# Optimization experiments

Measured on AMD Instinct MI355X. Metric: run time of the kernel, lower is better.

Reference implementation:

```python
import jax, jax.numpy as jnp
import numpy as np

N_NODES = 50000
N_EDGES = 800000
HIDDEN = 128
BN_EPS = 1e-5


def setup_inputs() -> dict:
    key = jax.random.key(0)
    k_h, k_e, k_wl, k_wr = jax.random.split(key, 4)
    h = jax.random.normal(k_h, (N_NODES, HIDDEN), dtype=jnp.float32)
    edge_index = jax.random.randint(k_e, (2, N_EDGES), 0, N_NODES, dtype=jnp.int32)
    W_l = jax.random.normal(k_wl, (HIDDEN, HIDDEN), dtype=jnp.float32) / np.sqrt(HIDDEN)
    b_l = jnp.zeros((HIDDEN,), dtype=jnp.float32)
    W_r = jax.random.normal(k_wr, (HIDDEN, HIDDEN), dtype=jnp.float32) / np.sqrt(HIDDEN)
    gamma = jnp.ones((HIDDEN,), dtype=jnp.float32)
    beta = jnp.zeros((HIDDEN,), dtype=jnp.float32)
    return {"h": h, "edge_index": edge_index, "W_l": W_l, "b_l": b_l,
            "W_r": W_r, "gamma": gamma, "beta": beta}


def reference(h, edge_index, W_l, b_l, W_r, gamma, beta):
    # SAGEConv(aggr='mean'): out_i = W_l @ mean_{j->i} h_j + b_l + W_r @ h_i
    src = edge_index[0]  # message sources
    dst = edge_index[1]  # message targets
    n = h.shape[0]
    msg_sum = jax.ops.segment_sum(h[src], dst, num_segments=n)          # [N, D]
    deg = jax.ops.segment_sum(jnp.ones_like(dst, dtype=h.dtype), dst, num_segments=n)
    agg = msg_sum / jnp.maximum(deg, 1.0)[:, None]                      # mean aggregation
    out = agg @ W_l.T + b_l + h @ W_r.T                                 # [N, D]
    # BatchNorm1d (training mode: batch statistics, biased variance)
    mean = jnp.mean(out, axis=0)
    var = jnp.var(out, axis=0)
    out = gamma * (out - mean) * jax.lax.rsqrt(var + BN_EPS) + beta
    out = jax.nn.relu(out)
    # dropout p=0.0 -> identity; residual add
    return out + h
```

## Files before the change

kernel.cpp:

```cpp
#include <hip/hip_runtime.h>

#define N_NODES 50000
#define N_EDGES 800000
#define HIDDEN  128
#define BN_EPS  1e-5f

typedef __attribute__((ext_vector_type(8))) short short8;
typedef __attribute__((ext_vector_type(8))) unsigned short ushort8;
typedef __attribute__((ext_vector_type(4))) float f32x4;

#define NBS 196

__device__ inline unsigned short f2bf(float x) {
    unsigned u = __float_as_uint(x);
    return (unsigned short)((u + 0x7FFFu + ((u >> 16) & 1u)) >> 16);
}
__device__ inline float bf2f(unsigned short u) {
    return __uint_as_float(((unsigned)u) << 16);
}
__device__ inline void cvt8(const float* x, short8& hi, short8& lo) {
#pragma unroll
    for (int i = 0; i < 8; i++) {
        unsigned u = __float_as_uint(x[i]);
        unsigned r = (u + 0x7FFFu + ((u >> 16) & 1u)) & 0xFFFF0000u;
        hi[i] = (short)(r >> 16);
        lo[i] = (short)f2bf(x[i] - __uint_as_float(r));
    }
}

#define NB_EDGE 3125
#define NB_HB   3125
#define NB_W    128

__global__ __launch_bounds__(256) void prep_kernel(
    const int* __restrict__ edge_index,
    const float* __restrict__ h,
    const float* __restrict__ W_l,
    const float* __restrict__ W_r,
    int* __restrict__ cnt,
    unsigned short* __restrict__ hb,
    unsigned short* __restrict__ WhiG,
    unsigned short* __restrict__ WloG,
    float* __restrict__ bn_acc)
{
    const int b = blockIdx.x;
    const int tid = threadIdx.x;
    if (b < NB_EDGE) {
        const int e = b * 256 + tid;
        atomicAdd(&cnt[edge_index[N_EDGES + e]], 1);
    } else if (b < NB_EDGE + NB_HB) {
        if (b == NB_EDGE) bn_acc[tid] = 0.0f;
        const size_t i8 = ((size_t)(b - NB_EDGE) * 256 + tid) * 8;
        const float4 p0 = *reinterpret_cast<const float4*>(h + i8);
        const float4 p1 = *reinterpret_cast<const float4*>(h + i8 + 4);
        ushort8 v;
        v[0] = f2bf(p0.x); v[1] = f2bf(p0.y); v[2] = f2bf(p0.z); v[3] = f2bf(p0.w);
        v[4] = f2bf(p1.x); v[5] = f2bf(p1.y); v[6] = f2bf(p1.z); v[7] = f2bf(p1.w);
        *reinterpret_cast<ushort8*>(hb + i8) = v;
    } else {
        const int gid = (b - NB_EDGE - NB_HB) * 256 + tid;
        const int n = gid >> 8;
        const int k = gid & 255;
        const float w = (k < 128) ? W_l[n * 128 + k] : W_r[n * 128 + (k - 128)];
        unsigned u = __float_as_uint(w);
        unsigned r = (u + 0x7FFFu + ((u >> 16) & 1u)) & 0xFFFF0000u;
        WhiG[gid] = (unsigned short)(r >> 16);
        WloG[gid] = f2bf(w - __uint_as_float(r));
    }
}

__global__ __launch_bounds__(256) void scan1_kernel(
    const int* __restrict__ cnt,
    int* __restrict__ bsum)
{
    const int t = threadIdx.x;
    const int idx = blockIdx.x * 256 + t;
    int v = (idx < N_NODES) ? cnt[idx] : 0;
    __shared__ int ps[256];
    ps[t] = v;
    __syncthreads();
    for (int off = 128; off > 0; off >>= 1) {
        if (t < off) ps[t] += ps[t + off];
        __syncthreads();
    }
    if (t == 0) bsum[blockIdx.x] = ps[0];
}

__global__ __launch_bounds__(256) void scan2_kernel(
    const int* __restrict__ bsum,
    int* __restrict__ boff,
    int* __restrict__ rp)
{
    const int t = threadIdx.x;
    int v = (t < NBS) ? bsum[t] : 0;
    __shared__ int ps[256];
    ps[t] = v;
    __syncthreads();
    for (int off = 1; off < 256; off <<= 1) {
        const int u = (t >= off) ? ps[t - off] : 0;
        __syncthreads();
        ps[t] += u;
        __syncthreads();
    }
    if (t < NBS) boff[t] = ps[t] - v;
    if (t == 255) rp[N_NODES] = ps[255];
}

__global__ __launch_bounds__(256) void scan3_kernel(
    const int* __restrict__ cnt,
    const int* __restrict__ boff,
    int* __restrict__ rp)
{
    const int t = threadIdx.x;
    const int idx = blockIdx.x * 256 + t;
    const int v = (idx < N_NODES) ? cnt[idx] : 0;
    __shared__ int ps[256];
    ps[t] = v;
    __syncthreads();
    for (int off = 1; off < 256; off <<= 1) {
        const int u = (t >= off) ? ps[t - off] : 0;
        __syncthreads();
        ps[t] += u;
        __syncthreads();
    }
    if (idx < N_NODES) rp[idx] = boff[blockIdx.x] + ps[t] - v;
}

__global__ __launch_bounds__(256) void place_kernel(
    const int* __restrict__ edge_index,
    const int* __restrict__ rp,
    int* __restrict__ cnt,
    unsigned short* __restrict__ csr)
{
    const int e = blockIdx.x * 256 + threadIdx.x;
    const int d = edge_index[N_EDGES + e];
    const int s = edge_index[e];
    const int pos = atomicSub(&cnt[d], 1) - 1;
    csr[rp[d] + pos] = (unsigned short)s;
}

__global__ __launch_bounds__(256) void gather_kernel(
    const unsigned short* __restrict__ hb,
    const int* __restrict__ rp,
    const unsigned short* __restrict__ csr,
    unsigned short* __restrict__ aggb)
{
    const int group = (threadIdx.x >> 4) & 3;
    const int sub   = threadIdx.x & 15;
    const int wave  = (blockIdx.x * 256 + threadIdx.x) >> 6;
    const int n = wave * 4 + group;
    if (n >= N_NODES) return;

    const int base = rp[n];
    const int c = rp[n + 1] - base;
    const int fo = sub * 8;

    float acc[8];
#pragma unroll
    for (int i = 0; i < 8; i++) acc[i] = 0.0f;

    int j = 0;
    for (; j + 4 <= c; j += 4) {
        const int s0 = csr[base + j],     s1 = csr[base + j + 1];
        const int s2 = csr[base + j + 2], s3 = csr[base + j + 3];
        const ushort8 v0 = *reinterpret_cast<const ushort8*>(hb + (size_t)s0 * HIDDEN + fo);
        const ushort8 v1 = *reinterpret_cast<const ushort8*>(hb + (size_t)s1 * HIDDEN + fo);
        const ushort8 v2 = *reinterpret_cast<const ushort8*>(hb + (size_t)s2 * HIDDEN + fo);
        const ushort8 v3 = *reinterpret_cast<const ushort8*>(hb + (size_t)s3 * HIDDEN + fo);
#pragma unroll
        for (int i = 0; i < 8; i++)
            acc[i] += (bf2f(v0[i]) + bf2f(v1[i])) + (bf2f(v2[i]) + bf2f(v3[i]));
    }
    for (; j < c; j++) {
        const ushort8 v0 = *reinterpret_cast<const ushort8*>(hb + (size_t)csr[base + j] * HIDDEN + fo);
#pragma unroll
        for (int i = 0; i < 8; i++) acc[i] += bf2f(v0[i]);
    }
    const float inv = 1.0f / (float)((c > 0) ? c : 1);
    ushort8 o;
#pragma unroll
    for (int i = 0; i < 8; i++) o[i] = f2bf(acc[i] * inv);
    *reinterpret_cast<ushort8*>(aggb + (size_t)n * HIDDEN + fo) = o;
}

__global__ __launch_bounds__(256) void gemm_kernel(
    const unsigned short* __restrict__ aggb,
    const float* __restrict__ h,
    const unsigned short* __restrict__ WhiG,
    const unsigned short* __restrict__ WloG,
    const float* __restrict__ b_l,
    float* __restrict__ out,
    float* __restrict__ bn_acc)
{
    __shared__ short WsH[128][64];
    __shared__ short WsL[128][64];
    __shared__ float bnS[128];
    __shared__ float bnS2[128];

    const int tid  = threadIdx.x;
    const int lane = tid & 63;
    const int wv   = tid >> 6;
    const int row0 = blockIdx.x * 128;
    const int colb = lane & 15;
    const int quad = lane >> 4;

    if (tid < 128) { bnS[tid] = 0.0f; bnS2[tid] = 0.0f; }

    f32x4 acc[2][8];
#pragma unroll
    for (int s = 0; s < 2; s++)
#pragma unroll
        for (int c = 0; c < 8; c++) acc[s][c] = (f32x4)(0.0f);

    const int wcol  = tid >> 1;
    const int sbase = (tid & 1) * 4;

    for (int kc = 0; kc < 4; kc++) {
        const int kb = (kc & 1) * 64;
        const int kw = kc * 64;

        __syncthreads();
#pragma unroll
        for (int j = 0; j < 4; j++) {
            const int slot = sbase + j;
            short8 vh = *reinterpret_cast<const short8*>(WhiG + (size_t)wcol * 256 + kw + slot * 8);
            short8 vl = *reinterpret_cast<const short8*>(WloG + (size_t)wcol * 256 + kw + slot * 8);
            const int sp = slot ^ (wcol & 7);
            *reinterpret_cast<short8*>(&WsH[wcol][sp * 8]) = vh;
            *reinterpret_cast<short8*>(&WsL[wcol][sp * 8]) = vl;
        }
        __syncthreads();

#pragma unroll
        for (int ks = 0; ks < 2; ks++) {
            short8 ahi[2], alo[2];
#pragma unroll
            for (int sub = 0; sub < 2; sub++) {
                int row = row0 + wv * 32 + sub * 16 + colb;
                row = (row < N_NODES) ? row : (N_NODES - 1);
                if (kc < 2) {
                    ahi[sub] = *reinterpret_cast<const short8*>(
                        aggb + (size_t)row * HIDDEN + kb + ks * 32 + quad * 8);
                } else {
                    const float* xp = h + (size_t)row * HIDDEN + kb + ks * 32 + quad * 8;
                    float xr[8];
                    const float4 p0 = *reinterpret_cast<const float4*>(xp);
                    const float4 p1 = *reinterpret_cast<const float4*>(xp + 4);
                    xr[0] = p0.x; xr[1] = p0.y; xr[2] = p0.z; xr[3] = p0.w;
                    xr[4] = p1.x; xr[5] = p1.y; xr[6] = p1.z; xr[7] = p1.w;
                    cvt8(xr, ahi[sub], alo[sub]);
                }
            }
#pragma unroll
            for (int c = 0; c < 8; c++) {
                const int bc = c * 16 + colb;
                const int sp = (ks * 4 + quad) ^ (bc & 7);
                short8 bhi = *reinterpret_cast<const short8*>(&WsH[bc][sp * 8]);
                short8 blo = *reinterpret_cast<const short8*>(&WsL[bc][sp * 8]);
#pragma unroll
                for (int sub = 0; sub < 2; sub++) {
                    acc[sub][c] = __builtin_amdgcn_mfma_f32_16x16x32_bf16(ahi[sub], bhi, acc[sub][c], 0, 0, 0);
                    acc[sub][c] = __builtin_amdgcn_mfma_f32_16x16x32_bf16(ahi[sub], blo, acc[sub][c], 0, 0, 0);
                    if (kc >= 2)
                        acc[sub][c] = __builtin_amdgcn_mfma_f32_16x16x32_bf16(alo[sub], bhi, acc[sub][c], 0, 0, 0);
                }
            }
        }
    }

#pragma unroll
    for (int c = 0; c < 8; c++) {
        const int col = c * 16 + colb;
        const float bias = b_l[col];
        float s = 0.0f, s2 = 0.0f;
#pragma unroll
        for (int sub = 0; sub < 2; sub++) {
            const int rbase = row0 + wv * 32 + sub * 16 + quad * 4;
#pragma unroll
            for (int reg = 0; reg < 4; reg++) {
                const int r = rbase + reg;
                if (r < N_NODES) {
                    const float o = acc[sub][c][reg] + bias;
                    out[(size_t)r * HIDDEN + col] = o;
                    s += o; s2 += o * o;
                }
            }
        }
        atomicAdd(&bnS[col], s);
        atomicAdd(&bnS2[col], s2);
    }
    __syncthreads();
    if (tid < 128) {
        atomicAdd(&bn_acc[tid], bnS[tid]);
        atomicAdd(&bn_acc[128 + tid], bnS2[tid]);
    }
}

__global__ __launch_bounds__(256) void bn_apply_kernel(
    const float* __restrict__ h,
    const float* __restrict__ gamma,
    const float* __restrict__ beta,
    const float* __restrict__ bn_acc,
    float* __restrict__ out)
{
    const float inv_n = 1.0f / (float)N_NODES;
    const size_t total = (size_t)N_NODES * HIDDEN;
    size_t idx = ((size_t)blockIdx.x * blockDim.x + threadIdx.x) * 4;
    const size_t stride = (size_t)gridDim.x * blockDim.x * 4;

    for (; idx < total; idx += stride) {
        const int col = (int)(idx & (HIDDEN - 1));
        float4 x  = *reinterpret_cast<float4*>(out + idx);
        float4 sm = *reinterpret_cast<const float4*>(bn_acc + col);
        float4 sq = *reinterpret_cast<const float4*>(bn_acc + HIDDEN + col);
        float4 g  = *reinterpret_cast<const float4*>(gamma + col);
        float4 bt = *reinterpret_cast<const float4*>(beta + col);
        float4 hr = *reinterpret_cast<const float4*>(h + idx);

        float4 res;
        {
            float m = sm.x * inv_n; float var = sq.x * inv_n - m * m;
            float v = g.x * (x.x - m) * rsqrtf(var + BN_EPS) + bt.x;
            res.x = fmaxf(v, 0.0f) + hr.x;
        }
        {
            float m = sm.y * inv_n; float var = sq.y * inv_n - m * m;
            float v = g.y * (x.y - m) * rsqrtf(var + BN_EPS) + bt.y;
            res.y = fmaxf(v, 0.0f) + hr.y;
        }
        {
            float m = sm.z * inv_n; float var = sq.z * inv_n - m * m;
            float v = g.z * (x.z - m) * rsqrtf(var + BN_EPS) + bt.z;
            res.z = fmaxf(v, 0.0f) + hr.z;
        }
        {
            float m = sm.w * inv_n; float var = sq.w * inv_n - m * m;
            float v = g.w * (x.w - m) * rsqrtf(var + BN_EPS) + bt.w;
            res.w = fmaxf(v, 0.0f) + hr.w;
        }
        *reinterpret_cast<float4*>(out + idx) = res;
    }
}

extern "C" void kernel_launch(void* const* d_in, const int* in_sizes, int n_in,
                              void* d_out, int out_size, void* d_ws, size_t ws_size,
                              hipStream_t stream)
{
    const float* h          = (const float*)d_in[0];
    const int*   edge_index = (const int*)d_in[1];
    const float* W_l        = (const float*)d_in[2];
    const float* b_l        = (const float*)d_in[3];
    const float* W_r        = (const float*)d_in[4];
    const float* gamma      = (const float*)d_in[5];
    const float* beta       = (const float*)d_in[6];
    float* out = (float*)d_out;

    char* ws = (char*)d_ws;
    int* cnt  = (int*)ws;
    int* rp   = cnt + 50000;
    int* bsum = rp + 50004;
    int* boff = bsum + 256;
    unsigned short* csr  = (unsigned short*)(boff + 256);
    unsigned short* hb   = csr + 800000;
    unsigned short* aggb = hb + 6400000;
    unsigned short* WhiG = aggb + 6400000;
    unsigned short* WloG = WhiG + 32768;
    float* bn_acc = (float*)(WloG + 32768);

    hipMemsetAsync(cnt, 0, 50000 * sizeof(int), stream);

    prep_kernel<<<NB_EDGE + NB_HB + NB_W, 256, 0, stream>>>(
        edge_index, h, W_l, W_r, cnt, hb, WhiG, WloG, bn_acc);

    scan1_kernel<<<NBS, 256, 0, stream>>>(cnt, bsum);
    scan2_kernel<<<1, 256, 0, stream>>>(bsum, boff, rp);
    scan3_kernel<<<NBS, 256, 0, stream>>>(cnt, boff, rp);

    place_kernel<<<NB_EDGE, 256, 0, stream>>>(edge_index, rp, cnt, csr);

    gather_kernel<<<(N_NODES / 4 + 3) / 4, 256, 0, stream>>>(hb, rp, csr, aggb);

    gemm_kernel<<<(N_NODES + 127) / 128, 256, 0, stream>>>(
        aggb, h, WhiG, WloG, b_l, out, bn_acc);

    bn_apply_kernel<<<2048, 256, 0, stream>>>(h, gamma, beta, bn_acc, out);
}
```

Measured before the change: 250.4 us.

## Fuse scan stages into one kernel and halve GEMM row tile per block

Merges the single-block block-offset scan and the per-block prefix scan into one kernel. Each block redundantly scans the 196 block sums, which removes one launch and the boff round trip through global memory. Also shrinks the GEMM tile from 128 to 64 rows per block, so each wave handles one 16-row subtile and the grid doubles to about 782 blocks. This improves occupancy and load balance on the many CUs, but doubles how often the weight tiles are staged into shared memory and the number of BN atomics.

```diff
diff --git a/kernel.cpp b/kernel.cpp
--- a/kernel.cpp
+++ b/kernel.cpp
@@ -86,32 +86,26 @@
     if (t == 0) bsum[blockIdx.x] = ps[0];
 }
 
-__global__ __launch_bounds__(256) void scan2_kernel(
+__global__ __launch_bounds__(256) void scan23_kernel(
+    const int* __restrict__ cnt,
     const int* __restrict__ bsum,
-    int* __restrict__ boff,
     int* __restrict__ rp)
 {
     const int t = threadIdx.x;
-    int v = (t < NBS) ? bsum[t] : 0;
-    __shared__ int ps[256];
-    ps[t] = v;
+    __shared__ int bs[256];
+    const int bv = (t < NBS) ? bsum[t] : 0;
+    bs[t] = bv;
     __syncthreads();
     for (int off = 1; off < 256; off <<= 1) {
-        const int u = (t >= off) ? ps[t - off] : 0;
-        __syncthreads();
-        ps[t] += u;
-        __syncthreads();
-    }
-    if (t < NBS) boff[t] = ps[t] - v;
-    if (t == 255) rp[N_NODES] = ps[255];
-}
-
-__global__ __launch_bounds__(256) void scan3_kernel(
-    const int* __restrict__ cnt,
-    const int* __restrict__ boff,
-    int* __restrict__ rp)
-{
-    const int t = threadIdx.x;
+        const int u = (t >= off) ? bs[t - off] : 0;
+        __syncthreads();
+        bs[t] += u;
+        __syncthreads();
+    }
+    if (blockIdx.x == 0 && t == 255) rp[N_NODES] = bs[255];
+    const int boff = bs[blockIdx.x] - bsum[blockIdx.x];
+    __syncthreads();
+
     const int idx = blockIdx.x * 256 + t;
     const int v = (idx < N_NODES) ? cnt[idx] : 0;
     __shared__ int ps[256];
@@ -123,7 +117,7 @@
         ps[t] += u;
         __syncthreads();
     }
-    if (idx < N_NODES) rp[idx] = boff[blockIdx.x] + ps[t] - v;
+    if (idx < N_NODES) rp[idx] = boff + ps[t] - v;
 }
 
 __global__ __launch_bounds__(256) void place_kernel(
@@ -200,17 +194,15 @@
     const int tid  = threadIdx.x;
     const int lane = tid & 63;
     const int wv   = tid >> 6;
-    const int row0 = blockIdx.x * 128;
+    const int row0 = blockIdx.x * 64;
     const int colb = lane & 15;
     const int quad = lane >> 4;
 
     if (tid < 128) { bnS[tid] = 0.0f; bnS2[tid] = 0.0f; }
 
-    f32x4 acc[2][8];
-#pragma unroll
-    for (int s = 0; s < 2; s++)
-#pragma unroll
-        for (int c = 0; c < 8; c++) acc[s][c] = (f32x4)(0.0f);
+    f32x4 acc[8];
+#pragma unroll
+    for (int c = 0; c < 8; c++) acc[c] = (f32x4)(0.0f);
 
     const int wcol  = tid >> 1;
     const int sbase = (tid & 1) * 4;
@@ -233,13 +225,12 @@
 
 #pragma unroll
         for (int ks = 0; ks < 2; ks++) {
-            short8 ahi[2], alo[2];
-#pragma unroll
-            for (int sub = 0; sub < 2; sub++) {
-                int row = row0 + wv * 32 + sub * 16 + colb;
+            short8 ahi, alo;
+            {
+                int row = row0 + wv * 16 + colb;
                 row = (row < N_NODES) ? row : (N_NODES - 1);
                 if (kc < 2) {
-                    ahi[sub] = *reinterpret_cast<const short8*>(
+                    ahi = *reinterpret_cast<const short8*>(
                         aggb + (size_t)row * HIDDEN + kb + ks * 32 + quad * 8);
                 } else {
                     const float* xp = h + (size_t)row * HIDDEN + kb + ks * 32 + quad * 8;
@@ -248,7 +239,7 @@
                     const float4 p1 = *reinterpret_cast<const float4*>(xp + 4);
                     xr[0] = p0.x; xr[1] = p0.y; xr[2] = p0.z; xr[3] = p0.w;
                     xr[4] = p1.x; xr[5] = p1.y; xr[6] = p1.z; xr[7] = p1.w;
-                    cvt8(xr, ahi[sub], alo[sub]);
+                    cvt8(xr, ahi, alo);
                 }
             }
 #pragma unroll
@@ -257,13 +248,10 @@
                 const int sp = (ks * 4 + quad) ^ (bc & 7);
                 short8 bhi = *reinterpret_cast<const short8*>(&WsH[bc][sp * 8]);
                 short8 blo = *reinterpret_cast<const short8*>(&WsL[bc][sp * 8]);
-#pragma unroll
-                for (int sub = 0; sub < 2; sub++) {
-                    acc[sub][c] = __builtin_amdgcn_mfma_f32_16x16x32_bf16(ahi[sub], bhi, acc[sub][c], 0, 0, 0);
-                    acc[sub][c] = __builtin_amdgcn_mfma_f32_16x16x32_bf16(ahi[sub], blo, acc[sub][c], 0, 0, 0);
-                    if (kc >= 2)
-                        acc[sub][c] = __builtin_amdgcn_mfma_f32_16x16x32_bf16(alo[sub], bhi, acc[sub][c], 0, 0, 0);
-                }
+                acc[c] = __builtin_amdgcn_mfma_f32_16x16x32_bf16(ahi, bhi, acc[c], 0, 0, 0);
+                acc[c] = __builtin_amdgcn_mfma_f32_16x16x32_bf16(ahi, blo, acc[c], 0, 0, 0);
+                if (kc >= 2)
+                    acc[c] = __builtin_amdgcn_mfma_f32_16x16x32_bf16(alo, bhi, acc[c], 0, 0, 0);
             }
         }
     }
@@ -273,17 +261,14 @@
         const int col = c * 16 + colb;
         const float bias = b_l[col];
         float s = 0.0f, s2 = 0.0f;
-#pragma unroll
-        for (int sub = 0; sub < 2; sub++) {
-            const int rbase = row0 + wv * 32 + sub * 16 + quad * 4;
-#pragma unroll
-            for (int reg = 0; reg < 4; reg++) {
-                const int r = rbase + reg;
-                if (r < N_NODES) {
-                    const float o = acc[sub][c][reg] + bias;
-                    out[(size_t)r * HIDDEN + col] = o;
-                    s += o; s2 += o * o;
-                }
+        const int rbase = row0 + wv * 16 + quad * 4;
+#pragma unroll
+        for (int reg = 0; reg < 4; reg++) {
+            const int r = rbase + reg;
+            if (r < N_NODES) {
+                const float o = acc[c][reg] + bias;
+                out[(size_t)r * HIDDEN + col] = o;
+                s += o; s2 += o * o;
             }
         }
         atomicAdd(&bnS[col], s);
@@ -373,14 +358,13 @@
         edge_index, h, W_l, W_r, cnt, hb, WhiG, WloG, bn_acc);
 
     scan1_kernel<<<NBS, 256, 0, stream>>>(cnt, bsum);
-    scan2_kernel<<<1, 256, 0, stream>>>(bsum, boff, rp);
-    scan3_kernel<<<NBS, 256, 0, stream>>>(cnt, boff, rp);
+    scan23_kernel<<<NBS, 256, 0, stream>>>(cnt, bsum, rp);
 
     place_kernel<<<NB_EDGE, 256, 0, stream>>>(edge_index, rp, cnt, csr);
 
     gather_kernel<<<(N_NODES / 4 + 3) / 4, 256, 0, stream>>>(hb, rp, csr, aggb);
 
-    gemm_kernel<<<(N_NODES + 127) / 128, 256, 0, stream>>>(
+    gemm_kernel<<<(N_NODES + 63) / 64, 256, 0, stream>>>(
         aggb, h, WhiG, WloG, b_l, out, bn_acc);
 
     bn_apply_kernel<<<2048, 256, 0, stream>>>(h, gamma, beta, bn_acc, out);
```

After: 269.4 us. +7.6%, slower.
